# Kernel optimization log

Hardware: AMD Instinct MI355X
Metric: run time of the kernel (lower is better)

Reference implementation:

```python
import jax, jax.numpy as jnp
import numpy as np

TOP_K = 8
N_TOKENS = 16384
D_MODEL = 4096
N_EXPERTS = 64


def setup_inputs() -> dict:
    key = jax.random.key(0)
    kx, kw = jax.random.split(key)
    x = jax.random.normal(kx, (N_TOKENS, D_MODEL), dtype=jnp.float32)
    # nn.Linear(input_dim, n_experts, bias=False): weight shape [n_experts, input_dim]
    W = jax.random.normal(kw, (N_EXPERTS, D_MODEL), dtype=jnp.float32) * (1.0 / np.sqrt(D_MODEL))
    return {"x": x, "W": W}


def reference(x, W):
    # logits = x @ W^T  -> [N_TOKENS, N_EXPERTS]
    logits = jnp.einsum('td,ed->te', x, W)
    # softmax in float32 (matches dtype=torch.float)
    probs = jax.nn.softmax(logits.astype(jnp.float32), axis=-1)
    # top-k expert indices per token -> [N_TOKENS, TOP_K] int32
    _, top_k_idx = jax.lax.top_k(probs, TOP_K)
    return top_k_idx
```

## Files before the change

kernel.cpp:

```cpp
#include <hip/hip_runtime.h>

typedef _Float16 f16x8 __attribute__((ext_vector_type(8)));
typedef float f32x16 __attribute__((ext_vector_type(16)));

#define NT 16384
#define DM 4096
#define NE 64
#define TOPK 8
#define BTOK 32
#define BK 64
#define NCHK (DM / BK)
#define XPL 4096
#define RSCALE 4.8828125e-4f
#define NEGINF (-3.402823466e38f)

#define MF(a, b, c) __builtin_amdgcn_mfma_f32_32x32x16_f16((a), (b), (c), 0, 0, 0)

#define SP(V, H, L, j) { const float _v = (V); const _Float16 _h = (_Float16)_v; \
  H[j] = _h; L[j] = (_Float16)((_v - (float)_h) * 2048.0f); }
#define SPLIT8(F0, F1, H, L) { \
  SP(F0.x, H, L, 0) SP(F0.y, H, L, 1) SP(F0.z, H, L, 2) SP(F0.w, H, L, 3) \
  SP(F1.x, H, L, 4) SP(F1.y, H, L, 5) SP(F1.z, H, L, 6) SP(F1.w, H, L, 7) }

__global__ __launch_bounds__(256) void wsplit_kernel(const float* __restrict__ W,
                                                     _Float16* __restrict__ wsp) {
  const int id = blockIdx.x * 256 + (int)threadIdx.x;
  const int e = id >> 9, kgg = id & 511;
  const float* src = W + (size_t)e * DM + kgg * 8;
  const float4 a = ((const float4*)src)[0];
  const float4 b = ((const float4*)src)[1];
  f16x8 H, L; SPLIT8(a, b, H, L)
  const int c = kgg >> 3, kg = kgg & 7;
  *(f16x8*)(wsp + ((size_t)(c * 2) * 512 + kg * 64 + e) * 8) = H;
  *(f16x8*)(wsp + ((size_t)(c * 2 + 1) * 512 + kg * 64 + e) * 8) = L;
}

template<bool PRE>
__global__ __launch_bounds__(256, 2) void gate_kernel(
    const float* __restrict__ x, const float* __restrict__ W,
    const _Float16* __restrict__ wsp, int* __restrict__ out) {

  __shared__ __align__(16) char xsmem[2][2 * XPL];
  __shared__ float lg[BTOK][68];

  const int t = (int)threadIdx.x;
  const int lane = t & 63;
  const int w = t >> 6;
  const int et = w & 1, kh = w >> 1;
  const int l31 = lane & 31, lhi = lane >> 5;
  const int kh4 = kh * 4;
  const int ecol = et * 32 + l31;
  const int tok0 = blockIdx.x * BTOK;

  const int sxtok = t >> 3, sxkg = t & 7;
  const float* xg = x + (size_t)(tok0 + sxtok) * DM + sxkg * 8;
  const int xoff0 = (sxkg * 32 + ((sxtok + sxkg) & 31)) * 16;

  const _Float16* wb = PRE ? (wsp + ((size_t)(kh4 + lhi) * 64 + ecol) * 8) : nullptr;
  const float* wf = W + (size_t)ecol * DM + (kh4 + lhi) * 8;

  f32x16 acc0 = {}, acc1 = {}, acc2 = {};

  float4 XA0, XA1, XB0, XB1;
  f16x8 B0h0, B0l0, B0h1, B0l1, B1h0, B1l0, B1h1, B1l1;

#define LOADX(c, Xp) { const float* _s = xg + (c) * BK; \
  Xp##0 = *(const float4*)_s; Xp##1 = *(const float4*)(_s + 4); }

#define LOADB(c, Bp) { \
  if (PRE) { \
    const _Float16* _q = wb + (size_t)(c) * 8192; \
    Bp##h0 = *(const f16x8*)(_q);          \
    Bp##h1 = *(const f16x8*)(_q + 1024);   \
    Bp##l0 = *(const f16x8*)(_q + 4096); \
    Bp##l1 = *(const f16x8*)(_q + 5120); \
  } else { \
    const float* _p = wf + (size_t)(c) * BK; \
    const float4 _a0 = ((const float4*)_p)[0], _a1 = ((const float4*)_p)[1]; \
    const float4 _b0 = ((const float4*)(_p + 16))[0], _b1 = ((const float4*)(_p + 16))[1]; \
    SPLIT8(_a0, _a1, Bp##h0, Bp##l0) \
    SPLIT8(_b0, _b1, Bp##h1, Bp##l1) \
  } }

#define WRX(bn, Xp) { \
  f16x8 XH, XL; SPLIT8(Xp##0, Xp##1, XH, XL) \
  char* _b = xsmem[bn]; \
  *(f16x8*)(_b + xoff0) = XH; \
  *(f16x8*)(_b + XPL + xoff0) = XL; }

#define KSTEP(bn, Bp, ks) { \
  const int _kg = kh4 + (ks) * 2 + lhi; \
  const int _ao = (_kg * 32 + ((l31 + _kg) & 31)) * 16; \
  const char* _b = xsmem[bn]; \
  const f16x8 ah = *(const f16x8*)(_b + _ao); \
  const f16x8 al = *(const f16x8*)(_b + XPL + _ao); \
  acc0 = MF(ah, Bp##h##ks, acc0); \
  acc1 = MF(ah, Bp##l##ks, acc1); \
  acc2 = MF(al, Bp##h##ks, acc2); }

#define BODY(c, Xw, Xl, Bc, Bn) { \
  if ((c) + 2 < NCHK) LOADX((c) + 2, Xl) \
  if ((c) + 1 < NCHK) LOADB((c) + 1, Bn) \
  KSTEP((c) & 1, Bc, 0) \
  KSTEP((c) & 1, Bc, 1) \
  if ((c) + 1 < NCHK) WRX(((c) + 1) & 1, Xw) \
  __syncthreads(); }

  LOADX(0, XA)
  WRX(0, XA)
  LOADB(0, B0)
  LOADX(1, XA)
  __syncthreads();

  for (int c = 0; c < NCHK; c += 2) {
    BODY(c,     XA, XB, B0, B1)
    BODY(c + 1, XB, XA, B1, B0)
  }

  float* mg = (float*)xsmem[0];
  if (kh == 1) {
#pragma unroll 16
    for (int i = 0; i < 16; ++i)
      mg[et * 1024 + i * 64 + lane] = acc0[i] + (acc1[i] + acc2[i]) * RSCALE;
  }
  __syncthreads();
  if (kh == 0) {
#pragma unroll 16
    for (int i = 0; i < 16; ++i) {
      const float v = acc0[i] + (acc1[i] + acc2[i]) * RSCALE
                    + mg[et * 1024 + i * 64 + lane];
      const int row = (i & 3) + ((i >> 2) << 3) + (lhi << 2);
      lg[row][ecol] = v;
    }
  }
  __syncthreads();

#define PICK(p) { \
  float m = v; \
  m = fmaxf(m, __shfl_xor(m, 32)); \
  m = fmaxf(m, __shfl_xor(m, 16)); \
  m = fmaxf(m, __shfl_xor(m, 8));  \
  m = fmaxf(m, __shfl_xor(m, 4));  \
  m = fmaxf(m, __shfl_xor(m, 2));  \
  m = fmaxf(m, __shfl_xor(m, 1));  \
  const unsigned long long bm = __ballot(v == m); \
  const int ii = (int)__builtin_ctzll(bm); \
  idx##p = ii; \
  v = (lane == ii) ? NEGINF : v; }

  for (int tt = 0; tt < 8; ++tt) {
    const int trow = w * 8 + tt;
    float v = lg[trow][lane];
    int idx0, idx1, idx2, idx3, idx4, idx5, idx6, idx7;
    PICK(0) PICK(1) PICK(2) PICK(3) PICK(4) PICK(5) PICK(6) PICK(7)
    if (lane == 0) {
      int4* op = (int4*)(out + (size_t)(tok0 + trow) * TOPK);
      op[0] = make_int4(idx0, idx1, idx2, idx3);
      op[1] = make_int4(idx4, idx5, idx6, idx7);
    }
  }
}

extern "C" void kernel_launch(void* const* d_in, const int* in_sizes, int n_in,
                              void* d_out, int out_size, void* d_ws, size_t ws_size,
                              hipStream_t stream) {
  const float* x = (const float*)d_in[0];
  const float* W = (const float*)d_in[1];
  int* out = (int*)d_out;
  (void)in_sizes; (void)n_in; (void)out_size;

  const size_t need = (size_t)NE * DM * 2 * sizeof(_Float16);
  if (ws_size >= need && d_ws != nullptr) {
    _Float16* wsp = (_Float16*)d_ws;
    hipLaunchKernelGGL(wsplit_kernel, dim3(128), dim3(256), 0, stream, W, wsp);
    hipLaunchKernelGGL((gate_kernel<true>), dim3(NT / BTOK), dim3(256),
                       0, stream, x, W, (const _Float16*)wsp, out);
  } else {
    hipLaunchKernelGGL((gate_kernel<false>), dim3(NT / BTOK), dim3(256),
                       0, stream, x, W, (const _Float16*)nullptr, out);
  }
}
```

Before: 90.73 us.

## Double K chunk and threads per block, split K across four wave pairs

Raises the K chunk from 64 to 128 and the block from 256 to 512 threads, so four wave pairs each take a quarter of every chunk, and the cross-wave reduction becomes a two-stage tree through shared memory. The two low-order correction accumulators are merged into one, freeing registers for the higher wave count. The top-k stage now spreads four tokens per wave across eight waves. The aim is more memory-level parallelism and fewer barriers per K. The cost is a larger shared-memory footprint, tighter register limits under launch_bounds(512,4), and extra reduction syncs.

```diff
diff --git a/kernel.cpp b/kernel.cpp
--- a/kernel.cpp
+++ b/kernel.cpp
@@ -8,9 +8,9 @@
 #define NE 64
 #define TOPK 8
 #define BTOK 32
-#define BK 64
+#define BK 128
 #define NCHK (DM / BK)
-#define XPL 4096
+#define XPL 8192
 #define RSCALE 4.8828125e-4f
 #define NEGINF (-3.402823466e38f)
 
@@ -30,13 +30,14 @@
   const float4 a = ((const float4*)src)[0];
   const float4 b = ((const float4*)src)[1];
   f16x8 H, L; SPLIT8(a, b, H, L)
-  const int c = kgg >> 3, kg = kgg & 7;
-  *(f16x8*)(wsp + ((size_t)(c * 2) * 512 + kg * 64 + e) * 8) = H;
-  *(f16x8*)(wsp + ((size_t)(c * 2 + 1) * 512 + kg * 64 + e) * 8) = L;
+  const int c = kgg >> 4, kg = kgg & 15;
+  _Float16* dst = wsp + ((size_t)(c * 2) * 1024 + kg * 64 + e) * 8;
+  *(f16x8*)dst = H;
+  *(f16x8*)(dst + 8192) = L;
 }
 
 template<bool PRE>
-__global__ __launch_bounds__(256, 2) void gate_kernel(
+__global__ __launch_bounds__(512, 4) void gate_kernel(
     const float* __restrict__ x, const float* __restrict__ W,
     const _Float16* __restrict__ wsp, int* __restrict__ out) {
 
@@ -46,20 +47,19 @@
   const int t = (int)threadIdx.x;
   const int lane = t & 63;
   const int w = t >> 6;
-  const int et = w & 1, kh = w >> 1;
+  const int et = w & 1, kq = w >> 1;
   const int l31 = lane & 31, lhi = lane >> 5;
-  const int kh4 = kh * 4;
   const int ecol = et * 32 + l31;
   const int tok0 = blockIdx.x * BTOK;
 
-  const int sxtok = t >> 3, sxkg = t & 7;
+  const int sxtok = t >> 4, sxkg = t & 15;
   const float* xg = x + (size_t)(tok0 + sxtok) * DM + sxkg * 8;
   const int xoff0 = (sxkg * 32 + ((sxtok + sxkg) & 31)) * 16;
 
-  const _Float16* wb = PRE ? (wsp + ((size_t)(kh4 + lhi) * 64 + ecol) * 8) : nullptr;
-  const float* wf = W + (size_t)ecol * DM + (kh4 + lhi) * 8;
-
-  f32x16 acc0 = {}, acc1 = {}, acc2 = {};
+  const _Float16* wb = PRE ? (wsp + ((size_t)(kq * 4 + lhi) * 64 + ecol) * 8) : nullptr;
+  const float* wf = W + (size_t)ecol * DM + (kq * 4 + lhi) * 8;
+
+  f32x16 acc0 = {}, acc1 = {};
 
   float4 XA0, XA1, XB0, XB1;
   f16x8 B0h0, B0l0, B0h1, B0l1, B1h0, B1l0, B1h1, B1l1;
@@ -69,11 +69,11 @@
 
 #define LOADB(c, Bp) { \
   if (PRE) { \
-    const _Float16* _q = wb + (size_t)(c) * 8192; \
-    Bp##h0 = *(const f16x8*)(_q);          \
-    Bp##h1 = *(const f16x8*)(_q + 1024);   \
-    Bp##l0 = *(const f16x8*)(_q + 4096); \
-    Bp##l1 = *(const f16x8*)(_q + 5120); \
+    const _Float16* _q = wb + (size_t)(c) * 16384; \
+    Bp##h0 = *(const f16x8*)(_q); \
+    Bp##h1 = *(const f16x8*)(_q + 1024);    \
+    Bp##l0 = *(const f16x8*)(_q + 8192);    \
+    Bp##l1 = *(const f16x8*)(_q + 9216); \
   } else { \
     const float* _p = wf + (size_t)(c) * BK; \
     const float4 _a0 = ((const float4*)_p)[0], _a1 = ((const float4*)_p)[1]; \
@@ -89,14 +89,14 @@
   *(f16x8*)(_b + XPL + xoff0) = XL; }
 
 #define KSTEP(bn, Bp, ks) { \
-  const int _kg = kh4 + (ks) * 2 + lhi; \
+  const int _kg = kq * 4 + (ks) * 2 + lhi; \
   const int _ao = (_kg * 32 + ((l31 + _kg) & 31)) * 16; \
   const char* _b = xsmem[bn]; \
   const f16x8 ah = *(const f16x8*)(_b + _ao); \
   const f16x8 al = *(const f16x8*)(_b + XPL + _ao); \
   acc0 = MF(ah, Bp##h##ks, acc0); \
   acc1 = MF(ah, Bp##l##ks, acc1); \
-  acc2 = MF(al, Bp##h##ks, acc2); }
+  acc1 = MF(al, Bp##h##ks, acc1); }
 
 #define BODY(c, Xw, Xl, Bc, Bn) { \
   if ((c) + 2 < NCHK) LOADX((c) + 2, Xl) \
@@ -117,18 +117,33 @@
     BODY(c + 1, XB, XA, B1, B0)
   }
 
-  float* mg = (float*)xsmem[0];
-  if (kh == 1) {
-#pragma unroll 16
-    for (int i = 0; i < 16; ++i)
-      mg[et * 1024 + i * 64 + lane] = acc0[i] + (acc1[i] + acc2[i]) * RSCALE;
-  }
-  __syncthreads();
-  if (kh == 0) {
+#pragma unroll 16
+  for (int i = 0; i < 16; ++i) acc0[i] += acc1[i] * RSCALE;
+
+  float* mg = (float*)xsmem;
+  if (kq == 1 || kq == 3) {
+    float* s = mg + (et * 2 + (kq >> 1)) * 1024;
+#pragma unroll 16
+    for (int i = 0; i < 16; ++i) s[i * 64 + lane] = acc0[i];
+  }
+  __syncthreads();
+  if (kq == 0 || kq == 2) {
+    const float* s = mg + (et * 2 + (kq >> 1)) * 1024;
+#pragma unroll 16
+    for (int i = 0; i < 16; ++i) acc0[i] += s[i * 64 + lane];
+  }
+  __syncthreads();
+  if (kq == 2) {
+    float* s = mg + (et * 2) * 1024;
+#pragma unroll 16
+    for (int i = 0; i < 16; ++i) s[i * 64 + lane] = acc0[i];
+  }
+  __syncthreads();
+  if (kq == 0) {
+    const float* s = mg + (et * 2) * 1024;
 #pragma unroll 16
     for (int i = 0; i < 16; ++i) {
-      const float v = acc0[i] + (acc1[i] + acc2[i]) * RSCALE
-                    + mg[et * 1024 + i * 64 + lane];
+      const float v = acc0[i] + s[i * 64 + lane];
       const int row = (i & 3) + ((i >> 2) << 3) + (lhi << 2);
       lg[row][ecol] = v;
     }
@@ -148,15 +163,19 @@
   idx##p = ii; \
   v = (lane == ii) ? NEGINF : v; }
 
-  for (int tt = 0; tt < 8; ++tt) {
-    const int trow = w * 8 + tt;
-    float v = lg[trow][lane];
-    int idx0, idx1, idx2, idx3, idx4, idx5, idx6, idx7;
-    PICK(0) PICK(1) PICK(2) PICK(3) PICK(4) PICK(5) PICK(6) PICK(7)
-    if (lane == 0) {
-      int4* op = (int4*)(out + (size_t)(tok0 + trow) * TOPK);
-      op[0] = make_int4(idx0, idx1, idx2, idx3);
-      op[1] = make_int4(idx4, idx5, idx6, idx7);
+  {
+    const int trow0 = w * 4;
+#pragma unroll
+    for (int tt = 0; tt < 4; ++tt) {
+      const int trow = trow0 + tt;
+      float v = lg[trow][lane];
+      int idx0, idx1, idx2, idx3, idx4, idx5, idx6, idx7;
+      PICK(0) PICK(1) PICK(2) PICK(3) PICK(4) PICK(5) PICK(6) PICK(7)
+      if (lane == 0) {
+        int4* op = (int4*)(out + (size_t)(tok0 + trow) * TOPK);
+        op[0] = make_int4(idx0, idx1, idx2, idx3);
+        op[1] = make_int4(idx4, idx5, idx6, idx7);
+      }
     }
   }
 }
@@ -173,10 +192,10 @@
   if (ws_size >= need && d_ws != nullptr) {
     _Float16* wsp = (_Float16*)d_ws;
     hipLaunchKernelGGL(wsplit_kernel, dim3(128), dim3(256), 0, stream, W, wsp);
-    hipLaunchKernelGGL((gate_kernel<true>), dim3(NT / BTOK), dim3(256),
+    hipLaunchKernelGGL((gate_kernel<true>), dim3(NT / BTOK), dim3(512),
                        0, stream, x, W, (const _Float16*)wsp, out);
   } else {
-    hipLaunchKernelGGL((gate_kernel<false>), dim3(NT / BTOK), dim3(256),
+    hipLaunchKernelGGL((gate_kernel<false>), dim3(NT / BTOK), dim3(512),
                        0, stream, x, W, (const _Float16*)nullptr, out);
   }
 }
```

Result: faster. 78.99 us (median of 2 runs) (-12.9%).
